# Optimization experiments

Measured on AMD Instinct MI355X. Metric: run time of the kernel, lower is better.

Reference implementation:

```python
import jax, jax.numpy as jnp
import numpy as np

S, B, T = 512, 512, 64

def setup_inputs() -> dict:
    key = jax.random.key(0)
    k1, k2, k3, k4, k5 = jax.random.split(key, 5)
    feats = jax.random.normal(k1, (S, B, T), dtype=jnp.float32)
    # contiguous-prefix masks with variable lengths in [S//2, S]
    lengths = jax.random.randint(k2, (B,), S // 2, S + 1)
    mask = (jnp.arange(S)[None, :] < lengths[:, None]).astype(jnp.float32)  # (B,S)
    u = lambda k, shp: jax.random.uniform(k, shp, jnp.float32, -0.1, 0.1)
    return {
        "feats": feats,
        "mask": mask,
        "start_transitions": u(k3, (T,)),
        "end_transitions": u(k4, (T,)),
        "transitions": u(k5, (T, T)),
    }

def reference(feats, mask, start_transitions, end_transitions, transitions):
    # feats: (S, B, T) emissions; mask: (B, S) 1/0 float, left-aligned
    s, b, t = feats.shape
    maskT = mask.T  # (S, B)

    score0 = start_transitions[None, :] + feats[0]  # (B, T)

    def step(vscore, inp):
        emis, m = inp  # (B,T), (B,)
        # score[b, i, j] = vscore[b,i] + trans[i,j] + emis[b,j]
        scores = vscore[:, :, None] + transitions[None, :, :] + emis[:, None, :]
        best = jnp.max(scores, axis=1)                       # (B, T)
        bp = jnp.argmax(scores, axis=1).astype(jnp.int32)    # (B, T) backpointers
        m1 = m[:, None]
        new_v = best * m1 + vscore * (1.0 - m1)
        return new_v, bp * m1.astype(jnp.int32)

    final_v, history = jax.lax.scan(step, score0, (feats[1:], maskT[1:]))
    final_v = final_v + end_transitions[None, :]
    last_path = jnp.argmax(final_v, axis=1).astype(jnp.int32)  # (B,)

    # append pad row of zeros -> history: (S, B, T)
    history = jnp.concatenate([history, jnp.zeros((1, b, t), jnp.int32)], axis=0)

    # insert last_path at position (length - 1) for every tag column
    lengths = jnp.sum(mask, axis=1).astype(jnp.int32)  # (B,)
    hb = history.transpose(1, 0, 2)                    # (B, S, T)
    hb = hb.at[jnp.arange(b), lengths - 1, :].set(last_path[:, None])
    history = hb.transpose(1, 0, 2)                    # (S, B, T)

    # backtrack: decode_idx[i] = history[i][b, last_path[b]], i = S-2 .. 0
    def back(lp, h):
        new = jnp.take_along_axis(h, lp[:, None], axis=1)[:, 0]
        return new, new

    _, dec = jax.lax.scan(back, last_path, history[:-1], reverse=True)  # (S-1, B)
    # decode_idx[S-1] is uninitialized in the torch code; fill with argmax last tag
    decode = jnp.concatenate([dec, last_path[None, :]], axis=0)  # (S, B)
    return decode.T  # (B, S)
```

## Files before the change

kernel.cpp:

```cpp
#include <hip/hip_runtime.h>

#define SS 512
#define BB 512
#define TT 64
#define NTHREADS 256

__global__ __launch_bounds__(NTHREADS) void viterbi_fused(
    const float* __restrict__ feats,
    const float* __restrict__ mask,
    const float* __restrict__ startt,
    const float* __restrict__ endt,
    const float* __restrict__ trans,
    int* __restrict__ out)
{
    __shared__ float vbuf[2][TT];
    __shared__ unsigned char hist[SS - 1][TT];
    __shared__ float redbuf[4];
    __shared__ int lenSh;

    const int b   = blockIdx.x;
    const int tid = threadIdx.x;
    const int j   = tid >> 2;
    const int li  = tid & 3;
    const int base_i = li * 16;
    const int wid = tid >> 6;
    const int lane = tid & 63;

    float msum = mask[b * SS + tid] + mask[b * SS + 256 + tid];
#pragma unroll
    for (int off = 1; off < 64; off <<= 1) msum += __shfl_xor(msum, off);
    if (lane == 0) redbuf[wid] = msum;
    __syncthreads();
    if (tid == 0) {
        float t = redbuf[0] + redbuf[1] + redbuf[2] + redbuf[3];
        lenSh = (int)(t + 0.5f);
    }

    float tc[16];
#pragma unroll
    for (int k = 0; k < 16; ++k) tc[k] = trans[(base_i + k) * TT + j];

    if (tid < TT) vbuf[0][tid] = startt[tid] + feats[(size_t)b * TT + tid];
    __syncthreads();

    const int len = lenSh;
    int p = 0;

    const float* fb = feats + (size_t)b * TT + j;
    float e_cur = fb[(size_t)1 * (BB * TT)];

    for (int s = 1; s < len; ++s) {
        const int sn = (s + 1 < SS) ? (s + 1) : s;
        float e_next = fb[(size_t)sn * (BB * TT)];

        float v[16];
#pragma unroll
        for (int q = 0; q < 4; ++q) {
            float4 t4 = *(const float4*)&vbuf[p][base_i + q * 4];
            v[q * 4 + 0] = t4.x; v[q * 4 + 1] = t4.y;
            v[q * 4 + 2] = t4.z; v[q * 4 + 3] = t4.w;
        }

        float best = -3.402823466e38f;
        int   bi   = base_i;
#pragma unroll
        for (int k = 0; k < 16; ++k) {
            float sc = (v[k] + tc[k]) + e_cur;
            if (sc > best) { best = sc; bi = base_i + k; }
        }

#pragma unroll
        for (int off = 1; off < 4; off <<= 1) {
            float ov = __shfl_xor(best, off);
            int   oi = __shfl_xor(bi, off);
            if (ov > best || (ov == best && oi < bi)) { best = ov; bi = oi; }
        }

        if (li == 0) {
            vbuf[p ^ 1][j] = best;
            hist[s - 1][j] = (unsigned char)bi;
        }
        __syncthreads();
        p ^= 1;
        e_cur = e_next;
    }

    if (tid < TT) {
        float fv = vbuf[p][tid] + endt[tid];
        int bix = tid;
#pragma unroll
        for (int off = 1; off < 64; off <<= 1) {
            float ov = __shfl_xor(fv, off);
            int   oi = __shfl_xor(bix, off);
            if (ov > fv || (ov == fv && oi < bix)) { fv = ov; bix = oi; }
        }
        if (tid == 0) {
            int* ob = out + (size_t)b * SS;
            int cur = bix;
            ob[SS - 1] = cur;
            ob[len - 1] = cur;
            for (int s2 = len - 2; s2 >= 0; --s2) {
                cur = hist[s2][cur];
                ob[s2] = cur;
            }
        }
    }

    for (int s2 = len + tid; s2 < SS - 1; s2 += NTHREADS)
        out[(size_t)b * SS + s2] = 0;
}

extern "C" void kernel_launch(void* const* d_in, const int* in_sizes, int n_in,
                              void* d_out, int out_size, void* d_ws, size_t ws_size,
                              hipStream_t stream) {
    const float* feats  = (const float*)d_in[0];
    const float* mask   = (const float*)d_in[1];
    const float* startt = (const float*)d_in[2];
    const float* endt   = (const float*)d_in[3];
    const float* trans  = (const float*)d_in[4];
    int* out = (int*)d_out;

    viterbi_fused<<<dim3(BB), dim3(NTHREADS), 0, stream>>>(
        feats, mask, startt, endt, trans, out);
}
```

Measured before the change: 279.0 us.

## Run each batch row's Viterbi in a single wavefront with register-held state

Each batch row now runs in a single 64-lane wavefront. Every lane holds one tag's score and a full transitions column in registers, and reads the other lanes' scores with readlane, which removes the shared-memory score buffer and the per-step block barrier. Emissions are prefetched eight steps ahead. The backtrack now keeps the current tag in registers and looks up the backpointer with a lane permute, instead of running serial shared-memory loads on one thread. The cost is 64 transition floats per lane (high register use), a serial 64-way max per lane, and one wave per block, which may lower latency hiding.

```diff
diff --git a/kernel.cpp b/kernel.cpp
--- a/kernel.cpp
+++ b/kernel.cpp
@@ -3,9 +3,9 @@
 #define SS 512
 #define BB 512
 #define TT 64
-#define NTHREADS 256
+#define FSTRIDE ((size_t)BB * TT)
 
-__global__ __launch_bounds__(NTHREADS) void viterbi_fused(
+__global__ __launch_bounds__(64, 1) void viterbi_wave(
     const float* __restrict__ feats,
     const float* __restrict__ mask,
     const float* __restrict__ startt,
@@ -13,101 +13,102 @@
     const float* __restrict__ trans,
     int* __restrict__ out)
 {
-    __shared__ float vbuf[2][TT];
-    __shared__ unsigned char hist[SS - 1][TT];
-    __shared__ float redbuf[4];
-    __shared__ int lenSh;
+    __shared__ unsigned char hist[(SS - 1) * TT];
 
-    const int b   = blockIdx.x;
-    const int tid = threadIdx.x;
-    const int j   = tid >> 2;
-    const int li  = tid & 3;
-    const int base_i = li * 16;
-    const int wid = tid >> 6;
-    const int lane = tid & 63;
+    const int b    = blockIdx.x;
+    const int lane = threadIdx.x;
 
-    float msum = mask[b * SS + tid] + mask[b * SS + 256 + tid];
+    float t[TT];
+#pragma unroll
+    for (int i = 0; i < TT; ++i) t[i] = trans[i * TT + lane];
+
+    float v = startt[lane] + feats[(size_t)b * TT + lane];
+
+    float msum = 0.f;
+#pragma unroll
+    for (int k = 0; k < 8; ++k) msum += mask[b * SS + lane + 64 * k];
 #pragma unroll
     for (int off = 1; off < 64; off <<= 1) msum += __shfl_xor(msum, off);
-    if (lane == 0) redbuf[wid] = msum;
-    __syncthreads();
-    if (tid == 0) {
-        float t = redbuf[0] + redbuf[1] + redbuf[2] + redbuf[3];
-        lenSh = (int)(t + 0.5f);
+    const int len = (int)(msum + 0.5f);
+
+    const float* fb = feats + (size_t)b * TT + lane;
+    unsigned hoff = lane;
+
+    auto body = [&](float e) {
+        float bc[4]; int xc[4];
+#pragma unroll
+        for (int c = 0; c < 4; ++c) {
+            float sv0 = __int_as_float(
+                __builtin_amdgcn_readlane(__float_as_int(v), 16 * c));
+            float bb = (sv0 + t[16 * c]) + e;
+            int   xx = 16 * c;
+#pragma unroll
+            for (int p = 1; p < 16; ++p) {
+                const int i = 16 * c + p;
+                float sv = __int_as_float(
+                    __builtin_amdgcn_readlane(__float_as_int(v), i));
+                float x = (sv + t[i]) + e;
+                if (x > bb) { bb = x; xx = i; }
+            }
+            bc[c] = bb; xc[c] = xx;
+        }
+        float bestv = bc[0]; int bi = xc[0];
+        if (bc[1] > bestv) { bestv = bc[1]; bi = xc[1]; }
+        if (bc[2] > bestv) { bestv = bc[2]; bi = xc[2]; }
+        if (bc[3] > bestv) { bestv = bc[3]; bi = xc[3]; }
+
+        v = bestv;
+        hist[hoff] = (unsigned char)bi;
+        hoff += TT;
+    };
+
+    float ec[8], en[8];
+#pragma unroll
+    for (int u = 0; u < 8; ++u) {
+        int sn = 1 + u; if (sn > SS - 1) sn = SS - 1;
+        ec[u] = fb[(size_t)sn * FSTRIDE];
     }
 
-    float tc[16];
+    int s = 1;
+    while (s + 8 <= len) {
 #pragma unroll
-    for (int k = 0; k < 16; ++k) tc[k] = trans[(base_i + k) * TT + j];
-
-    if (tid < TT) vbuf[0][tid] = startt[tid] + feats[(size_t)b * TT + tid];
-    __syncthreads();
-
-    const int len = lenSh;
-    int p = 0;
-
-    const float* fb = feats + (size_t)b * TT + j;
-    float e_cur = fb[(size_t)1 * (BB * TT)];
-
-    for (int s = 1; s < len; ++s) {
-        const int sn = (s + 1 < SS) ? (s + 1) : s;
-        float e_next = fb[(size_t)sn * (BB * TT)];
-
-        float v[16];
+        for (int u = 0; u < 8; ++u) {
+            int sn = s + 8 + u; if (sn > SS - 1) sn = SS - 1;
+            en[u] = fb[(size_t)sn * FSTRIDE];
+        }
 #pragma unroll
-        for (int q = 0; q < 4; ++q) {
-            float4 t4 = *(const float4*)&vbuf[p][base_i + q * 4];
-            v[q * 4 + 0] = t4.x; v[q * 4 + 1] = t4.y;
-            v[q * 4 + 2] = t4.z; v[q * 4 + 3] = t4.w;
-        }
-
-        float best = -3.402823466e38f;
-        int   bi   = base_i;
+        for (int u = 0; u < 8; ++u) body(ec[u]);
 #pragma unroll
-        for (int k = 0; k < 16; ++k) {
-            float sc = (v[k] + tc[k]) + e_cur;
-            if (sc > best) { best = sc; bi = base_i + k; }
-        }
-
+        for (int u = 0; u < 8; ++u) ec[u] = en[u];
+        s += 8;
+    }
 #pragma unroll
-        for (int off = 1; off < 4; off <<= 1) {
-            float ov = __shfl_xor(best, off);
-            int   oi = __shfl_xor(bi, off);
-            if (ov > best || (ov == best && oi < bi)) { best = ov; bi = oi; }
-        }
-
-        if (li == 0) {
-            vbuf[p ^ 1][j] = best;
-            hist[s - 1][j] = (unsigned char)bi;
-        }
-        __syncthreads();
-        p ^= 1;
-        e_cur = e_next;
+    for (int u = 0; u < 7; ++u) {
+        if (s + u < len) body(ec[u]);
     }
 
-    if (tid < TT) {
-        float fv = vbuf[p][tid] + endt[tid];
-        int bix = tid;
+    float fv = v + endt[lane];
+    int bix = lane;
 #pragma unroll
-        for (int off = 1; off < 64; off <<= 1) {
-            float ov = __shfl_xor(fv, off);
-            int   oi = __shfl_xor(bix, off);
-            if (ov > fv || (ov == fv && oi < bix)) { fv = ov; bix = oi; }
-        }
-        if (tid == 0) {
-            int* ob = out + (size_t)b * SS;
-            int cur = bix;
-            ob[SS - 1] = cur;
-            ob[len - 1] = cur;
-            for (int s2 = len - 2; s2 >= 0; --s2) {
-                cur = hist[s2][cur];
-                ob[s2] = cur;
-            }
-        }
+    for (int off = 1; off < 64; off <<= 1) {
+        float ov = __shfl_xor(fv, off);
+        int   oi = __shfl_xor(bix, off);
+        if (ov > fv || (ov == fv && oi < bix)) { fv = ov; bix = oi; }
     }
+    int cur = bix;
+    int* ob = out + (size_t)b * SS;
 
-    for (int s2 = len + tid; s2 < SS - 1; s2 += NTHREADS)
-        out[(size_t)b * SS + s2] = 0;
+    if (lane == 0) { ob[SS - 1] = cur; ob[len - 1] = cur; }
+
+    for (int s2 = len + lane; s2 < SS - 1; s2 += TT) ob[s2] = 0;
+
+    int rowb = hist[(len - 2) * TT + lane];
+    for (int s2 = len - 2; s2 >= 0; --s2) {
+        int rown = (s2 > 0) ? hist[(s2 - 1) * TT + lane] : 0;
+        cur = __builtin_amdgcn_ds_bpermute(cur << 2, rowb);
+        if (lane == 0) ob[s2] = cur;
+        rowb = rown;
+    }
 }
 
 extern "C" void kernel_launch(void* const* d_in, const int* in_sizes, int n_in,
@@ -120,6 +121,6 @@
     const float* trans  = (const float*)d_in[4];
     int* out = (int*)d_out;
 
-    viterbi_fused<<<dim3(BB), dim3(NTHREADS), 0, stream>>>(
+    viterbi_wave<<<dim3(BB), dim3(TT), 0, stream>>>(
         feats, mask, startt, endt, trans, out);
 }
```

Measured after the change: 386.3 us. 38.5% more time.
